# Optimization experiments

Measured on AMD Instinct MI355X. Metric: run time of the kernel, lower is better.

Reference implementation:

```python
import jax, jax.numpy as jnp
import numpy as np

B, N, C = 64, 257, 768
H, HD = 12, 64  # num_heads, head_dim
WH, WW = 16, 16
SCALE = HD ** -0.5


def make_rel_pos_index(Wh, Ww):
    coords = np.stack(np.meshgrid(np.arange(Wh), np.arange(Ww), indexing='ij'))  # [2,Wh,Ww]
    cf = coords.reshape(2, -1)                      # [2, Wh*Ww]
    rc = cf[:, :, None] - cf[:, None, :]            # [2, N-1, N-1]
    rc = rc.transpose(1, 2, 0).copy()               # [N-1, N-1, 2]
    rc[:, :, 0] += Wh - 1
    rc[:, :, 1] += Ww - 1
    rc[:, :, 0] *= 2 * Ww - 1
    nrd = (2 * Wh - 1) * (2 * Ww - 1) + 3
    idx = np.zeros((Wh * Ww + 1, Wh * Ww + 1), dtype=np.int32)
    idx[1:, 1:] = rc.sum(-1)
    idx[0, :] = nrd - 3
    idx[:, 0] = nrd - 2
    idx[0, 0] = nrd - 1
    return jnp.asarray(idx)


def setup_inputs() -> dict:
    key = jax.random.key(0)
    ks = jax.random.split(key, 7)
    nrd = (2 * WH - 1) * (2 * WW - 1) + 3  # 964
    return {
        'x': jax.random.normal(ks[0], (B, N, C), jnp.float32),
        'qkv_w': jax.random.normal(ks[1], (3 * C, C), jnp.float32) * 0.02,
        'q_bias': jax.random.normal(ks[2], (C,), jnp.float32) * 0.02,
        'v_bias': jax.random.normal(ks[3], (C,), jnp.float32) * 0.02,
        'rpb_table': jax.random.normal(ks[4], (nrd, H), jnp.float32) * 0.02,
        'proj_w': jax.random.normal(ks[5], (C, C), jnp.float32) * 0.02,
        'proj_b': jax.random.normal(ks[6], (C,), jnp.float32) * 0.02,
        'rel_pos_index': make_rel_pos_index(WH, WW),
    }


def reference(x, qkv_w, q_bias, v_bias, rpb_table, proj_w, proj_b, rel_pos_index):
    b, n, c = x.shape
    # qkv bias: [q_bias, zeros(k), v_bias]
    qkv_bias = jnp.concatenate([q_bias, jnp.zeros_like(v_bias), v_bias])
    qkv = x @ qkv_w.T + qkv_bias                         # [B,N,3C]
    qkv = qkv.reshape(b, n, 3, H, HD).transpose(2, 0, 3, 1, 4)  # [3,B,H,N,HD]
    q, k, v = qkv[0], qkv[1], qkv[2]
    q = q * SCALE
    attn = jnp.einsum('bhnd,bhmd->bhnm', q, k)           # [B,H,N,N]
    # relative position bias gather: [N,N,H] -> [H,N,N]
    bias = rpb_table[rel_pos_index.reshape(-1)].reshape(n, n, H).transpose(2, 0, 1)
    attn = attn + bias[None]
    # fp32 softmax, cast back to q dtype
    attn = jax.nn.softmax(attn.astype(jnp.float32), axis=-1).astype(q.dtype)
    out = jnp.einsum('bhnm,bhmd->bhnd', attn, v)         # [B,H,N,HD]
    out = out.transpose(0, 2, 1, 3).reshape(b, n, H * HD)
    return out @ proj_w.T + proj_b
```

## Files before the change

kernel.cpp:

```cpp
#include <hip/hip_runtime.h>
#include <hip/hip_bf16.h>
#include <stdint.h>

typedef __bf16 bf16_t;
typedef __bf16 bf16x8 __attribute__((ext_vector_type(8)));
typedef float  f32x4  __attribute__((ext_vector_type(4)));

static constexpr int BB  = 64;
static constexpr int NN  = 257;
static constexpr int CC  = 768;
static constexpr int HH  = 12;
static constexpr int M   = BB * NN;
static constexpr int NP  = 288;
static constexpr int KLD = 72;
static constexpr int VLD = 328;
static constexpr int PLD = 296;
static constexpr int BJT = 24;
static constexpr float QSCALE = 0.125f;

static constexpr size_t OFF_XB   = 0;
static constexpr size_t SZ_XB    = (size_t)M * CC * 2;
static constexpr size_t OFF_WQKV = OFF_XB + SZ_XB;
static constexpr size_t SZ_WQKV  = (size_t)3 * CC * CC * 2;
static constexpr size_t OFF_WPRJ = OFF_WQKV + SZ_WQKV;
static constexpr size_t SZ_WPRJ  = (size_t)CC * CC * 2;
static constexpr size_t OFF_Q    = OFF_WPRJ + SZ_WPRJ;
static constexpr size_t SZ_Q     = (size_t)BB * HH * NP * 64 * 2;
static constexpr size_t OFF_K    = OFF_Q + SZ_Q;
static constexpr size_t SZ_K     = (size_t)BB * HH * NP * KLD * 2;
static constexpr size_t OFF_V    = OFF_K + SZ_K;
static constexpr size_t SZ_V     = (size_t)BB * HH * 64 * VLD * 2;
static constexpr size_t OFF_BIAS = OFF_V + SZ_V;
static constexpr size_t SZ_BIAS  = (size_t)HH * NP * 16 * BJT * 2;
static constexpr size_t OFF_AO   = OFF_BIAS + SZ_BIAS;
static constexpr size_t SZ_AO    = (size_t)M * CC * 2;

__device__ __forceinline__ void load_lds16(const bf16_t* g, bf16_t* l) {
  __builtin_amdgcn_global_load_lds(
      (const __attribute__((address_space(1))) uint32_t*)g,
      (__attribute__((address_space(3))) uint32_t*)l, 16, 0, 0);
}

__global__ void prep_kernel(const float* __restrict__ x, const float* __restrict__ qkv_w,
                            const float* __restrict__ proj_w, const float* __restrict__ rpb,
                            const int* __restrict__ rpi,
                            bf16_t* __restrict__ xb, bf16_t* __restrict__ wqkv,
                            bf16_t* __restrict__ wprj, bf16_t* __restrict__ biasb,
                            bf16_t* __restrict__ kz, bf16_t* __restrict__ vz) {
  const int NX4  = M * CC / 4;
  const int NW14 = 3 * CC * CC / 4;
  const int NW24 = CC * CC / 4;
  const int NBI  = HH * NP * 16 * BJT;
  const int NPK  = BB * HH * 31 * KLD;
  const int NPV  = BB * HH * 64 * 71;
  const int total = NX4 + NW14 + NW24 + NBI + NPK + NPV;
  for (int u = blockIdx.x * blockDim.x + threadIdx.x; u < total;
       u += gridDim.x * blockDim.x) {
    if (u < NX4) {
      float4 v = ((const float4*)x)[u];
      union { ushort4 us; bf16_t b[4]; } cv;
      cv.b[0] = (bf16_t)v.x; cv.b[1] = (bf16_t)v.y;
      cv.b[2] = (bf16_t)v.z; cv.b[3] = (bf16_t)v.w;
      ((ushort4*)xb)[u] = cv.us;
    } else if (u < NX4 + NW14) {
      int t = u - NX4;
      float4 v = ((const float4*)qkv_w)[t];
      union { ushort4 us; bf16_t b[4]; } cv;
      cv.b[0] = (bf16_t)v.x; cv.b[1] = (bf16_t)v.y;
      cv.b[2] = (bf16_t)v.z; cv.b[3] = (bf16_t)v.w;
      ((ushort4*)wqkv)[t] = cv.us;
    } else if (u < NX4 + NW14 + NW24) {
      int t = u - NX4 - NW14;
      float4 v = ((const float4*)proj_w)[t];
      union { ushort4 us; bf16_t b[4]; } cv;
      cv.b[0] = (bf16_t)v.x; cv.b[1] = (bf16_t)v.y;
      cv.b[2] = (bf16_t)v.z; cv.b[3] = (bf16_t)v.w;
      ((ushort4*)wprj)[t] = cv.us;
    } else if (u < NX4 + NW14 + NW24 + NBI) {
      int t  = u - NX4 - NW14 - NW24;
      int jt = t % BJT;
      int c  = (t / BJT) & 15;
      int q  = (t / (BJT * 16)) % NP;
      int h  = t / (BJT * 16 * NP);
      int key = jt * 16 + c;
      float val;
      if (jt >= 18)           val = 0.0f;
      else if (key < NN && q < NN) val = rpb[rpi[q * NN + key] * HH + h];
      else                    val = (key >= NN) ? -1e30f : 0.0f;
      biasb[t] = (bf16_t)val;
    } else if (u < NX4 + NW14 + NW24 + NBI + NPK) {
      int t = u - NX4 - NW14 - NW24 - NBI;
      int c = t % KLD;
      int r = (t / KLD) % 31;
      int bh = t / (KLD * 31);
      kz[((size_t)bh * NP + 257 + r) * KLD + c] = (bf16_t)0.0f;
    } else {
      int t = u - NX4 - NW14 - NW24 - NBI - NPK;
      int c = t % 71;
      int rf = t / 71;
      vz[(size_t)rf * VLD + 257 + c] = (bf16_t)0.0f;
    }
  }
}

template <int MODE, int GN>
__global__ __launch_bounds__(512) void gemm_kernel(
    const bf16_t* __restrict__ A, const bf16_t* __restrict__ Bt,
    const float* __restrict__ bias0, const float* __restrict__ bias1,
    bf16_t* __restrict__ qo, bf16_t* __restrict__ ko, bf16_t* __restrict__ vo,
    float* __restrict__ fo) {
  __shared__ bf16_t smem[24576];
  bf16_t* Alds = smem;
  bf16_t* Blds = smem + 8192;

  const int nwg = gridDim.x, orig = blockIdx.x;
  const int qq = nwg >> 3, rr8 = nwg & 7;
  const int xcd = orig & 7, local = orig >> 3;
  const int wg = (xcd < rr8 ? xcd * (qq + 1) : rr8 * (qq + 1) + (xcd - rr8) * qq) + local;
  const int tm = wg / GN, tn = wg % GN;

  const int tid = threadIdx.x;
  const int w = tid >> 6, lane = tid & 63;
  const int wm = w >> 2, wn = w & 3;
  const int g = lane >> 4, cq = lane & 15;
  const int c7 = cq & 7;
  const int lr8 = lane >> 3;
  const int stgc = ((lane & 7) ^ (lane >> 3)) << 3;
  f32x4 acc[4][4] = {};

  for (int kt = 0; kt < 12; ++kt) {
    __syncthreads();
#pragma unroll
    for (int j = 0; j < 2; ++j) {
      int r = j * 64 + w * 8 + lr8;
      int arow = tm * 128 + r;
      arow = (arow < M) ? arow : (M - 1);
      load_lds16(A + (size_t)arow * CC + kt * 64 + stgc, &Alds[(j * 64 + w * 8) * 64]);
    }
#pragma unroll
    for (int j = 0; j < 4; ++j) {
      int r = j * 64 + w * 8 + lr8;
      int brow = tn * 256 + r;
      load_lds16(Bt + (size_t)brow * CC + kt * 64 + stgc, &Blds[(j * 64 + w * 8) * 64]);
    }
    __syncthreads();
#pragma unroll
    for (int ks = 0; ks < 2; ++ks) {
      bf16x8 af[4], bfr[4];
#pragma unroll
      for (int mi = 0; mi < 4; ++mi)
        af[mi] = *(const bf16x8*)&Alds[(wm * 64 + mi * 16 + cq) * 64 +
                                       ((((ks << 2) | g) ^ c7) << 3)];
#pragma unroll
      for (int ni = 0; ni < 4; ++ni)
        bfr[ni] = *(const bf16x8*)&Blds[(wn * 64 + ni * 16 + cq) * 64 +
                                        ((((ks << 2) | g) ^ c7) << 3)];
#pragma unroll
      for (int mi = 0; mi < 4; ++mi)
#pragma unroll
        for (int ni = 0; ni < 4; ++ni)
          acc[mi][ni] = __builtin_amdgcn_mfma_f32_16x16x32_bf16(
              af[mi], bfr[ni], acc[mi][ni], 0, 0, 0);
    }
  }

  if (MODE == 0 && tn >= 6) {
    __syncthreads();
    bf16_t* scr = &smem[w * 2048];
    const int tokBase = tm * 128 + wm * 64;
    const int m2 = tokBase + lane;
    const bool mok = m2 < M;
    const int b2 = mok ? m2 / NN : 0;
    const int nn2 = mok ? (m2 - b2 * NN) : 0;
    const int cbase = (tn - 6) * 256 + wn * 64;
#pragma unroll
    for (int ni = 0; ni < 4; ++ni) {
      float bsum = bias1[cbase + ni * 16 + cq];
#pragma unroll
      for (int mi = 0; mi < 4; ++mi)
#pragma unroll
        for (int r = 0; r < 4; ++r)
          scr[(mi * 16 + 4 * g + r) * 21 + cq] = (bf16_t)(acc[mi][ni][r] + bsum);
      asm volatile("s_waitcnt lgkmcnt(0)" ::: "memory");
      __builtin_amdgcn_sched_barrier(0);
      if (mok) {
#pragma unroll
        for (int ch = 0; ch < 16; ++ch) {
          bf16_t v = scr[lane * 21 + ch];
          int c2 = cbase + ni * 16 + ch;
          int h = c2 >> 6, hd = c2 & 63;
          vo[((size_t)(b2 * HH + h) * 64 + hd) * VLD + nn2] = v;
        }
      }
      asm volatile("s_waitcnt lgkmcnt(0)" ::: "memory");
      __builtin_amdgcn_sched_barrier(0);
    }
  } else {
#pragma unroll
    for (int mi = 0; mi < 4; ++mi) {
#pragma unroll
      for (int r = 0; r < 4; ++r) {
        int m = tm * 128 + wm * 64 + mi * 16 + 4 * g + r;
        if (m >= M) continue;
        int bidx = m / NN, nn = m % NN;
#pragma unroll
        for (int ni = 0; ni < 4; ++ni) {
          int cg = tn * 256 + wn * 64 + ni * 16 + cq;
          float v = acc[mi][ni][r];
          if (MODE == 0) {
            if (cg < CC) {
              int h = cg >> 6, hd = cg & 63;
              qo[((size_t)(bidx * HH + h) * NP + nn) * 64 + hd] =
                  (bf16_t)((v + bias0[cg]) * QSCALE);
            } else {
              int c2 = cg - CC; int h = c2 >> 6, hd = c2 & 63;
              ko[((size_t)(bidx * HH + h) * NP + nn) * KLD + hd] = (bf16_t)v;
            }
          } else {
            fo[(size_t)m * CC + cg] = v + bias0[cg];
          }
        }
      }
    }
  }
}

__global__ __launch_bounds__(512, 1) void attn_kernel(
    const bf16_t* __restrict__ qg, const bf16_t* __restrict__ kg,
    const bf16_t* __restrict__ vg, const bf16_t* __restrict__ biasb,
    bf16_t* __restrict__ outb) {
  __shared__ bf16_t shm[79872];
  const int bh = blockIdx.x;
  const int b = bh / HH, h = bh % HH;
  const int w = threadIdx.x >> 6, lane = threadIdx.x & 63;
  const int g = lane >> 4, cq = lane & 15;
  const bf16_t* qp = qg + (size_t)bh * NP * 64;
  const bf16_t* kp = kg + (size_t)bh * NP * KLD;
  const bf16_t* vp = vg + (size_t)bh * 64 * VLD;
  const bf16_t* bp = biasb + (size_t)h * NP * 16 * BJT;
  bf16_t* Klds = shm;
  bf16_t* Vlds = shm + 20992;
  bf16_t* pl   = shm + 41984 + w * (16 * PLD);

  for (int i = w; i < 82; i += 8) {
    if (i < 41) load_lds16(kp + i * 512 + lane * 8, Klds + i * 512);
    else        load_lds16(vp + (i - 41) * 512 + lane * 8, Vlds + (i - 41) * 512);
  }
  asm volatile("s_waitcnt vmcnt(0)" ::: "memory");
  __syncthreads();

  for (int qt = w; qt < 17; qt += 8) {
    bf16x8 aq0 = *(const bf16x8*)&qp[(qt * 16 + cq) * 64 + 8 * g];
    bf16x8 aq1 = *(const bf16x8*)&qp[(qt * 16 + cq) * 64 + 32 + 8 * g];

    f32x4 s[18];
#pragma unroll
    for (int r = 0; r < 4; ++r) {
      const bf16_t* bb = &bp[((qt * 16 + 4 * g + r) * 16 + cq) * BJT];
      bf16x8 b0 = *(const bf16x8*)(bb);
      bf16x8 b1 = *(const bf16x8*)(bb + 8);
      bf16x8 b2 = *(const bf16x8*)(bb + 16);
#pragma unroll
      for (int jt = 0; jt < 8; ++jt)  s[jt][r] = (float)b0[jt];
#pragma unroll
      for (int jt = 8; jt < 16; ++jt) s[jt][r] = (float)b1[jt - 8];
      s[16][r] = (float)b2[0];
      s[17][r] = (float)b2[1];
    }

#pragma unroll
    for (int jt = 0; jt < 18; ++jt) {
      bf16x8 kb0 = *(const bf16x8*)&Klds[(jt * 16 + cq) * KLD + 8 * g];
      bf16x8 kb1 = *(const bf16x8*)&Klds[(jt * 16 + cq) * KLD + 32 + 8 * g];
      s[jt] = __builtin_amdgcn_mfma_f32_16x16x32_bf16(aq0, kb0, s[jt], 0, 0, 0);
      s[jt] = __builtin_amdgcn_mfma_f32_16x16x32_bf16(aq1, kb1, s[jt], 0, 0, 0);
    }

    float inv[4];
#pragma unroll
    for (int r = 0; r < 4; ++r) {
      float mx = s[0][r];
#pragma unroll
      for (int jt = 1; jt < 18; ++jt) mx = fmaxf(mx, s[jt][r]);
      mx = fmaxf(mx, __shfl_xor(mx, 1, 16));
      mx = fmaxf(mx, __shfl_xor(mx, 2, 16));
      mx = fmaxf(mx, __shfl_xor(mx, 4, 16));
      mx = fmaxf(mx, __shfl_xor(mx, 8, 16));
      float sum = 0.f;
#pragma unroll
      for (int jt = 0; jt < 18; ++jt) {
        float e = __expf(s[jt][r] - mx);
        s[jt][r] = e;
        sum += e;
      }
      sum += __shfl_xor(sum, 1, 16);
      sum += __shfl_xor(sum, 2, 16);
      sum += __shfl_xor(sum, 4, 16);
      sum += __shfl_xor(sum, 8, 16);
      inv[r] = 1.0f / sum;
    }

#pragma unroll
    for (int jt = 0; jt < 18; ++jt)
#pragma unroll
      for (int r = 0; r < 4; ++r)
        pl[(4 * g + r) * PLD + jt * 16 + cq] = (bf16_t)s[jt][r];
    __asm__ volatile("s_waitcnt lgkmcnt(0)" ::: "memory");
    __builtin_amdgcn_sched_barrier(0);

    f32x4 o[4] = {};
#pragma unroll
    for (int kk = 0; kk < 9; ++kk) {
      bf16x8 pa = *(const bf16x8*)&pl[cq * PLD + kk * 32 + 8 * g];
#pragma unroll
      for (int nt = 0; nt < 4; ++nt) {
        bf16x8 vb = *(const bf16x8*)&Vlds[(nt * 16 + cq) * VLD + kk * 32 + 8 * g];
        o[nt] = __builtin_amdgcn_mfma_f32_16x16x32_bf16(pa, vb, o[nt], 0, 0, 0);
      }
    }

#pragma unroll
    for (int r = 0; r < 4; ++r) {
      int q = qt * 16 + 4 * g + r;
      if (q < NN) {
        float iv = inv[r];
#pragma unroll
        for (int nt = 0; nt < 4; ++nt)
          outb[((size_t)b * NN + q) * CC + h * 64 + nt * 16 + cq] =
              (bf16_t)(o[nt][r] * iv);
      }
    }
  }
}

extern "C" void kernel_launch(void* const* d_in, const int* in_sizes, int n_in,
                              void* d_out, int out_size, void* d_ws, size_t ws_size,
                              hipStream_t stream) {
  const float* x      = (const float*)d_in[0];
  const float* qkv_w  = (const float*)d_in[1];
  const float* q_bias = (const float*)d_in[2];
  const float* v_bias = (const float*)d_in[3];
  const float* rpb    = (const float*)d_in[4];
  const float* proj_w = (const float*)d_in[5];
  const float* proj_b = (const float*)d_in[6];
  const int*   rpi    = (const int*)d_in[7];

  char* ws = (char*)d_ws;
  bf16_t* xb    = (bf16_t*)(ws + OFF_XB);
  bf16_t* wqkv  = (bf16_t*)(ws + OFF_WQKV);
  bf16_t* wprj  = (bf16_t*)(ws + OFF_WPRJ);
  bf16_t* qo    = (bf16_t*)(ws + OFF_Q);
  bf16_t* ko    = (bf16_t*)(ws + OFF_K);
  bf16_t* vo    = (bf16_t*)(ws + OFF_V);
  bf16_t* biasb = (bf16_t*)(ws + OFF_BIAS);
  bf16_t* ao    = (bf16_t*)(ws + OFF_AO);
  float*  out   = (float*)d_out;

  prep_kernel<<<2048, 256, 0, stream>>>(x, qkv_w, proj_w, rpb, rpi,
                                        xb, wqkv, wprj, biasb, ko, vo);
  gemm_kernel<0, 9><<<129 * 9, 512, 0, stream>>>(xb, wqkv, q_bias, v_bias,
                                                 qo, ko, vo, nullptr);
  attn_kernel<<<768, 512, 0, stream>>>(qo, ko, vo, biasb, ao);
  gemm_kernel<1, 3><<<129 * 3, 512, 0, stream>>>(ao, wprj, proj_b, nullptr,
                                                 nullptr, nullptr, nullptr, out);
}
```

Baseline: 194.4 us.

## Fuse fp32-to-bf16 conversion of x into QKV GEMM A-tile loads

Removes the separate conversion of x into a bf16 workspace buffer in the prep kernel. The QKV GEMM now reads fp32 x directly, converts it in registers and writes bf16 into LDS, avoiding a full write and re-read of the bf16 copy. The padding zero-fill for K and V is also vectorised to 16-byte stores. As a trade-off, the A loads become synchronous register loads rather than direct-to-LDS loads, and every N-tile re-reads x in fp32, doubling A-side global traffic per tile.

Result: faster. 187.9 us (-3.3%).

```diff
diff --git a/kernel.cpp b/kernel.cpp
--- a/kernel.cpp
+++ b/kernel.cpp
@@ -18,9 +18,7 @@
 static constexpr int BJT = 24;
 static constexpr float QSCALE = 0.125f;
 
-static constexpr size_t OFF_XB   = 0;
-static constexpr size_t SZ_XB    = (size_t)M * CC * 2;
-static constexpr size_t OFF_WQKV = OFF_XB + SZ_XB;
+static constexpr size_t OFF_WQKV = 0;
 static constexpr size_t SZ_WQKV  = (size_t)3 * CC * CC * 2;
 static constexpr size_t OFF_WPRJ = OFF_WQKV + SZ_WQKV;
 static constexpr size_t SZ_WPRJ  = (size_t)CC * CC * 2;
@@ -41,71 +39,62 @@
       (__attribute__((address_space(3))) uint32_t*)l, 16, 0, 0);
 }
 
-__global__ void prep_kernel(const float* __restrict__ x, const float* __restrict__ qkv_w,
-                            const float* __restrict__ proj_w, const float* __restrict__ rpb,
+__global__ void prep_kernel(const float* __restrict__ qkv_w,
+                            const float* __restrict__ proj_w,
+                            const float* __restrict__ rpb,
                             const int* __restrict__ rpi,
-                            bf16_t* __restrict__ xb, bf16_t* __restrict__ wqkv,
-                            bf16_t* __restrict__ wprj, bf16_t* __restrict__ biasb,
+                            bf16_t* __restrict__ wqkv, bf16_t* __restrict__ wprj,
+                            bf16_t* __restrict__ biasb,
                             bf16_t* __restrict__ kz, bf16_t* __restrict__ vz) {
-  const int NX4  = M * CC / 4;
   const int NW14 = 3 * CC * CC / 4;
   const int NW24 = CC * CC / 4;
   const int NBI  = HH * NP * 16 * BJT;
-  const int NPK  = BB * HH * 31 * KLD;
-  const int NPV  = BB * HH * 64 * 71;
-  const int total = NX4 + NW14 + NW24 + NBI + NPK + NPV;
+  const int NPK2 = BB * HH * 279;
+  const int NPV2 = BB * HH * 64 * 9;
+  const int total = NW14 + NW24 + NBI + NPK2 + NPV2;
+  const uint4 zz = {0u, 0u, 0u, 0u};
   for (int u = blockIdx.x * blockDim.x + threadIdx.x; u < total;
        u += gridDim.x * blockDim.x) {
-    if (u < NX4) {
-      float4 v = ((const float4*)x)[u];
+    if (u < NW14) {
+      float4 v = ((const float4*)qkv_w)[u];
       union { ushort4 us; bf16_t b[4]; } cv;
       cv.b[0] = (bf16_t)v.x; cv.b[1] = (bf16_t)v.y;
       cv.b[2] = (bf16_t)v.z; cv.b[3] = (bf16_t)v.w;
-      ((ushort4*)xb)[u] = cv.us;
-    } else if (u < NX4 + NW14) {
-      int t = u - NX4;
-      float4 v = ((const float4*)qkv_w)[t];
-      union { ushort4 us; bf16_t b[4]; } cv;
-      cv.b[0] = (bf16_t)v.x; cv.b[1] = (bf16_t)v.y;
-      cv.b[2] = (bf16_t)v.z; cv.b[3] = (bf16_t)v.w;
-      ((ushort4*)wqkv)[t] = cv.us;
-    } else if (u < NX4 + NW14 + NW24) {
-      int t = u - NX4 - NW14;
+      ((ushort4*)wqkv)[u] = cv.us;
+    } else if (u < NW14 + NW24) {
+      int t = u - NW14;
       float4 v = ((const float4*)proj_w)[t];
       union { ushort4 us; bf16_t b[4]; } cv;
       cv.b[0] = (bf16_t)v.x; cv.b[1] = (bf16_t)v.y;
       cv.b[2] = (bf16_t)v.z; cv.b[3] = (bf16_t)v.w;
       ((ushort4*)wprj)[t] = cv.us;
-    } else if (u < NX4 + NW14 + NW24 + NBI) {
-      int t  = u - NX4 - NW14 - NW24;
+    } else if (u < NW14 + NW24 + NBI) {
+      int t  = u - NW14 - NW24;
       int jt = t % BJT;
       int c  = (t / BJT) & 15;
       int q  = (t / (BJT * 16)) % NP;
       int h  = t / (BJT * 16 * NP);
       int key = jt * 16 + c;
       float val;
-      if (jt >= 18)           val = 0.0f;
+      if (jt >= 18)                val = 0.0f;
       else if (key < NN && q < NN) val = rpb[rpi[q * NN + key] * HH + h];
-      else                    val = (key >= NN) ? -1e30f : 0.0f;
+      else                         val = (key >= NN) ? -1e30f : 0.0f;
       biasb[t] = (bf16_t)val;
-    } else if (u < NX4 + NW14 + NW24 + NBI + NPK) {
-      int t = u - NX4 - NW14 - NW24 - NBI;
-      int c = t % KLD;
-      int r = (t / KLD) % 31;
-      int bh = t / (KLD * 31);
-      kz[((size_t)bh * NP + 257 + r) * KLD + c] = (bf16_t)0.0f;
+    } else if (u < NW14 + NW24 + NBI + NPK2) {
+      int t = u - NW14 - NW24 - NBI;
+      int bh = t / 279, c = t - bh * 279;
+      *(uint4*)(kz + (size_t)bh * NP * KLD + 257 * KLD + c * 8) = zz;
     } else {
-      int t = u - NX4 - NW14 - NW24 - NBI - NPK;
-      int c = t % 71;
-      int rf = t / 71;
-      vz[(size_t)rf * VLD + 257 + c] = (bf16_t)0.0f;
+      int t = u - NW14 - NW24 - NBI - NPK2;
+      int row = t / 9, c = t - row * 9;
+      *(uint4*)(vz + (size_t)row * VLD + 256 + c * 8) = zz;
     }
   }
 }
 
 template <int MODE, int GN>
 __global__ __launch_bounds__(512) void gemm_kernel(
-    const bf16_t* __restrict__ A, const bf16_t* __restrict__ Bt,
+    const void* __restrict__ Ain, const bf16_t* __restrict__ Bt,
     const float* __restrict__ bias0, const float* __restrict__ bias1,
     bf16_t* __restrict__ qo, bf16_t* __restrict__ ko, bf16_t* __restrict__ vo,
     float* __restrict__ fo) {
@@ -131,17 +120,30 @@
   for (int kt = 0; kt < 12; ++kt) {
     __syncthreads();
 #pragma unroll
+    for (int j = 0; j < 4; ++j) {
+      int r = j * 64 + w * 8 + lr8;
+      int brow = tn * 256 + r;
+      load_lds16(Bt + (size_t)brow * CC + kt * 64 + stgc, &Blds[(j * 64 + w * 8) * 64]);
+    }
+#pragma unroll
     for (int j = 0; j < 2; ++j) {
       int r = j * 64 + w * 8 + lr8;
       int arow = tm * 128 + r;
       arow = (arow < M) ? arow : (M - 1);
-      load_lds16(A + (size_t)arow * CC + kt * 64 + stgc, &Alds[(j * 64 + w * 8) * 64]);
-    }
-#pragma unroll
-    for (int j = 0; j < 4; ++j) {
-      int r = j * 64 + w * 8 + lr8;
-      int brow = tn * 256 + r;
-      load_lds16(Bt + (size_t)brow * CC + kt * 64 + stgc, &Blds[(j * 64 + w * 8) * 64]);
+      if (MODE == 0) {
+        const float* src = (const float*)Ain + (size_t)arow * CC + kt * 64 + stgc;
+        float4 v0 = ((const float4*)src)[0];
+        float4 v1 = ((const float4*)src)[1];
+        bf16x8 pk;
+        pk[0] = (bf16_t)v0.x; pk[1] = (bf16_t)v0.y;
+        pk[2] = (bf16_t)v0.z; pk[3] = (bf16_t)v0.w;
+        pk[4] = (bf16_t)v1.x; pk[5] = (bf16_t)v1.y;
+        pk[6] = (bf16_t)v1.z; pk[7] = (bf16_t)v1.w;
+        *(bf16x8*)&Alds[(j * 64 + w * 8) * 64 + lane * 8] = pk;
+      } else {
+        load_lds16((const bf16_t*)Ain + (size_t)arow * CC + kt * 64 + stgc,
+                   &Alds[(j * 64 + w * 8) * 64]);
+      }
     }
     __syncthreads();
 #pragma unroll
@@ -346,7 +348,6 @@
   const int*   rpi    = (const int*)d_in[7];
 
   char* ws = (char*)d_ws;
-  bf16_t* xb    = (bf16_t*)(ws + OFF_XB);
   bf16_t* wqkv  = (bf16_t*)(ws + OFF_WQKV);
   bf16_t* wprj  = (bf16_t*)(ws + OFF_WPRJ);
   bf16_t* qo    = (bf16_t*)(ws + OFF_Q);
@@ -356,11 +357,13 @@
   bf16_t* ao    = (bf16_t*)(ws + OFF_AO);
   float*  out   = (float*)d_out;
 
-  prep_kernel<<<2048, 256, 0, stream>>>(x, qkv_w, proj_w, rpb, rpi,
-                                        xb, wqkv, wprj, biasb, ko, vo);
-  gemm_kernel<0, 9><<<129 * 9, 512, 0, stream>>>(xb, wqkv, q_bias, v_bias,
+  prep_kernel<<<2048, 256, 0, stream>>>(qkv_w, proj_w, rpb, rpi,
+                                        wqkv, wprj, biasb, ko, vo);
+  gemm_kernel<0, 9><<<129 * 9, 512, 0, stream>>>((const void*)x, wqkv,
+                                                 q_bias, v_bias,
                                                  qo, ko, vo, nullptr);
   attn_kernel<<<768, 512, 0, stream>>>(qo, ko, vo, biasb, ao);
-  gemm_kernel<1, 3><<<129 * 3, 512, 0, stream>>>(ao, wprj, proj_b, nullptr,
+  gemm_kernel<1, 3><<<129 * 3, 512, 0, stream>>>((const void*)ao, wprj,
+                                                 proj_b, nullptr,
                                                  nullptr, nullptr, nullptr, out);
 }
```
